# Optimization experiments

Hardware: AMD Instinct MI355X
Metric: run time of the kernel (lower is better)

The kernel has to match this reference:

```python
import jax, jax.numpy as jnp
import numpy as np

B, S, D, E, F, K = 2, 4096, 1024, 8, 2048, 2


def setup_inputs() -> dict:
    key = jax.random.key(0)
    k1, k2, k3, k4 = jax.random.split(key, 4)
    return {
        "inputs_raw": jax.random.normal(k1, (B, S, D), dtype=jnp.float32),
        "gate_w": jax.random.normal(k2, (D, E), dtype=jnp.float32) * (D ** -0.5),
        "w1": jax.random.normal(k3, (E, D, F), dtype=jnp.float32) * (D ** -0.5),
        "w2": jax.random.normal(k4, (E, F, D), dtype=jnp.float32) * (F ** -0.5),
        "top_k": K,
    }


def reference(inputs_raw, gate_w, w1, w2, top_k):
    ishape = inputs_raw.shape
    x = inputs_raw.reshape(-1, ishape[-1])                 # [T, D]
    n_experts = gate_w.shape[-1]

    # --- gating: top-k logits, softmax over the selected k (float32, like the torch code) ---
    logits = x @ gate_w                                    # [T, E]
    top_vals, top_idx = jax.lax.top_k(logits, top_k)       # [T, K]
    top_w = jax.nn.softmax(top_vals.astype(jnp.float32), axis=-1).astype(x.dtype)
    # dense combine weights [T, E]; zero for unselected experts
    combine = jnp.einsum("tk,tke->te", top_w,
                         jax.nn.one_hot(top_idx, n_experts, dtype=x.dtype))

    # --- experts: D -> F (SiLU) -> D, evaluated densely and combined with gate weights ---
    h = jax.nn.silu(jnp.einsum("td,edf->etf", x, w1))      # [E, T, F]
    y = jnp.einsum("etf,efd->etd", h, w2)                  # [E, T, D]
    out = jnp.einsum("te,etd->td", combine, y)             # [T, D]
    return out.reshape(ishape)
```

## Files before the change

kernel.cpp:

```cpp
#include <hip/hip_runtime.h>
#include <cstdint>
#include <cstddef>

#define T_TOK 8192
#define DIM   1024
#define NE    8
#define FF    2048
#define TOPK  2

typedef __bf16 bf16x8 __attribute__((ext_vector_type(8)));
typedef float  floatx4 __attribute__((ext_vector_type(4)));

__device__ __forceinline__ unsigned short f2bf(float f) {
  unsigned int u = __float_as_uint(f);
  unsigned int r = 0x7FFFu + ((u >> 16) & 1u);
  return (unsigned short)((u + r) >> 16);
}

__device__ __forceinline__ void gl_lds16(const void* g, void* l) {
  __builtin_amdgcn_global_load_lds(
      (__attribute__((address_space(1))) void*)g,
      (__attribute__((address_space(3))) void*)l,
      16, 0, 0);
}

__global__ __launch_bounds__(256) void transpose_bf16_kernel(
    const float* __restrict__ in, unsigned short* __restrict__ out,
    int R, int C)
{
  __shared__ float tile[32][33];
  int e  = blockIdx.z;
  int c0 = blockIdx.x * 32, r0 = blockIdx.y * 32;
  int tx = threadIdx.x & 31, ty = threadIdx.x >> 5;
  const float* inp = in + (size_t)e * R * C;
  unsigned short* op = out + (size_t)e * R * C;
  for (int i = 0; i < 4; ++i)
    tile[ty + i * 8][tx] = inp[(size_t)(r0 + ty + i * 8) * C + c0 + tx];
  __syncthreads();
  for (int i = 0; i < 4; ++i)
    op[(size_t)(c0 + ty + i * 8) * R + r0 + tx] = f2bf(tile[tx][ty + i * 8]);
}

__global__ __launch_bounds__(256) void gate_kernel(
    const float* __restrict__ x, const float* __restrict__ gw,
    unsigned short* __restrict__ xb, int* __restrict__ tokExp,
    float* __restrict__ tokW)
{
  __shared__ float gwT[NE][DIM];
  int tid = threadIdx.x;
  for (int i = tid; i < DIM * NE; i += 256) {
    int d = i >> 3, e = i & 7;
    gwT[e][d] = gw[i];
  }
  __syncthreads();

  int wv = tid >> 6, lane = tid & 63;
  int t = blockIdx.x * 4 + wv;
  const float* xrow = x + (size_t)t * DIM;
  unsigned short* xbrow = xb + (size_t)t * DIM;

  double acc[NE];
  for (int e = 0; e < NE; ++e) acc[e] = 0.0;

  for (int j = 0; j < 4; ++j) {
    float4 xv = ((const float4*)xrow)[j * 64 + lane];
    ushort4 s;
    s.x = f2bf(xv.x); s.y = f2bf(xv.y); s.z = f2bf(xv.z); s.w = f2bf(xv.w);
    ((ushort4*)xbrow)[j * 64 + lane] = s;
    double xd0 = (double)xv.x, xd1 = (double)xv.y;
    double xd2 = (double)xv.z, xd3 = (double)xv.w;
    for (int e = 0; e < NE; ++e) {
      float4 g = ((const float4*)&gwT[e][0])[j * 64 + lane];
      acc[e] += xd0 * (double)g.x + xd1 * (double)g.y +
                xd2 * (double)g.z + xd3 * (double)g.w;
    }
  }

  for (int s = 32; s > 0; s >>= 1)
    for (int e = 0; e < NE; ++e)
      acc[e] += __shfl_down(acc[e], s, 64);

  if (lane == 0) {
    int e0 = 0; double v0 = acc[0];
    for (int e = 1; e < NE; ++e) if (acc[e] > v0) { v0 = acc[e]; e0 = e; }
    int e1 = -1; double v1 = -1.0e300;
    for (int e = 0; e < NE; ++e) {
      if (e == e0) continue;
      if (acc[e] > v1) { v1 = acc[e]; e1 = e; }
    }
    float a = (float)v0, b = (float)v1;
    float eb = __expf(b - a);
    float den = 1.0f + eb;
    tokExp[t] = e0 | (e1 << 8);
    tokW[2 * t + 0] = 1.0f / den;
    tokW[2 * t + 1] = eb / den;
  }
}

__global__ __launch_bounds__(64) void assign_kernel(
    const int* __restrict__ tokExp, int* __restrict__ tokEnc,
    int* __restrict__ tIdx, int* __restrict__ cnt, int* __restrict__ off)
{
  int lane = threadIdx.x;
  unsigned long long below = (1ull << lane) - 1ull;
  int base[NE];
  for (int e = 0; e < NE; ++e) base[e] = 0;

  for (int it = 0; it < T_TOK / 64; ++it) {
    int t = it * 64 + lane;
    int enc = tokExp[t];
    int e0 = enc & 0xFF, e1 = (enc >> 8) & 0xFF;
    int s0 = 0, s1 = 0;
    for (int e = 0; e < NE; ++e) {
      unsigned long long m0 = __ballot(e0 == e);
      unsigned long long m1 = __ballot(e1 == e);
      if (e0 == e) s0 = base[e] + __popcll(m0 & below);
      if (e1 == e) s1 = base[e] + __popcll(m0) + __popcll(m1 & below);
      base[e] += __popcll(m0) + __popcll(m1);
    }
    tokEnc[2 * t + 0] = (e0 << 16) | s0;
    tokEnc[2 * t + 1] = (e1 << 16) | s1;
    tIdx[e0 * T_TOK + s0] = t;
    tIdx[e1 * T_TOK + s1] = t;
  }

  if (lane == 0) {
    int a = 0;
    for (int e = 0; e < NE; ++e) { cnt[e] = base[e]; off[e] = a; a += base[e]; }
    off[NE] = a;
  }
}

__global__ __launch_bounds__(256, 4) void gemm1_kernel(
    const unsigned short* __restrict__ xb,
    const unsigned short* __restrict__ w1t,
    unsigned short* __restrict__ h,
    const int* __restrict__ tIdx, const int* __restrict__ cnt,
    const int* __restrict__ off)
{
  int g = blockIdx.x;
  int e = g & 7;
  int b = g >> 3;
  int phase = b >> 9;
  int m = (b >> 3) & 63;
  int nl = b & 7;
  int count = cnt[e];
  int r0 = m * 128;
  if (r0 >= count) return;
  int n0 = (phase * 8 + nl) * 128;

  __shared__ __align__(16) unsigned short As[8][128][8];
  __shared__ __align__(16) unsigned short Bs[8][128][8];

  int tid = threadIdx.x, lane = tid & 63, w = tid >> 6;
  int wr = w >> 1, wc = w & 1;
  int quad = lane >> 4, li = lane & 15;

  const unsigned short* ag[2];
  const unsigned short* bg[2];
  for (int c = 0; c < 2; ++c) {
    int mm = c * 64 + lane;
    int r = r0 + mm; if (r > count - 1) r = count - 1;
    ag[c] = xb + (size_t)tIdx[e * T_TOK + r] * DIM;
    bg[c] = w1t + ((size_t)e * FF + (n0 + mm)) * DIM;
  }

  floatx4 acc[4][4];
  for (int mi = 0; mi < 4; ++mi)
    for (int ni = 0; ni < 4; ++ni)
      for (int q = 0; q < 4; ++q) acc[mi][ni][q] = 0.0f;

  for (int k0 = 0; k0 < DIM; k0 += 64) {
    __syncthreads();
    for (int kk = 0; kk < 2; ++kk) {
      int kq = w + kk * 4;
      gl_lds16(ag[0] + k0 + kq * 8, &As[kq][0][0]);
      gl_lds16(ag[1] + k0 + kq * 8, &As[kq][64][0]);
      gl_lds16(bg[0] + k0 + kq * 8, &Bs[kq][0][0]);
      gl_lds16(bg[1] + k0 + kq * 8, &Bs[kq][64][0]);
    }
    __syncthreads();
    for (int ks = 0; ks < 2; ++ks) {
      bf16x8 af[4], bf[4];
      for (int mi = 0; mi < 4; ++mi)
        af[mi] = *(const bf16x8*)&As[ks * 4 + quad][wr * 64 + mi * 16 + li][0];
      for (int ni = 0; ni < 4; ++ni)
        bf[ni] = *(const bf16x8*)&Bs[ks * 4 + quad][wc * 64 + ni * 16 + li][0];
      for (int mi = 0; mi < 4; ++mi)
        for (int ni = 0; ni < 4; ++ni)
          acc[mi][ni] = __builtin_amdgcn_mfma_f32_16x16x32_bf16(
              af[mi], bf[ni], acc[mi][ni], 0, 0, 0);
    }
  }

  size_t hb = (size_t)off[e];
  for (int mi = 0; mi < 4; ++mi) {
    int rowb = wr * 64 + mi * 16 + quad * 4;
    for (int rr = 0; rr < 4; ++rr) {
      int r = r0 + rowb + rr;
      if (r >= count) continue;
      unsigned short* hrow = h + (hb + r) * FF + n0 + wc * 64 + li;
      for (int ni = 0; ni < 4; ++ni) {
        float v = acc[mi][ni][rr];
        float s = v / (1.0f + __expf(-v));
        hrow[ni * 16] = f2bf(s);
      }
    }
  }
}

__global__ __launch_bounds__(256, 4) void gemm2_kernel(
    const unsigned short* __restrict__ h,
    const unsigned short* __restrict__ w2t,
    float* __restrict__ yv,
    const int* __restrict__ cnt, const int* __restrict__ off)
{
  int g = blockIdx.x;
  int e = g & 7;
  int b = g >> 3;
  int phase = b >> 8;
  int m = (b >> 2) & 63;
  int nl = b & 3;
  int count = cnt[e];
  int r0 = m * 128;
  if (r0 >= count) return;
  int n0 = (phase * 4 + nl) * 128;

  __shared__ __align__(16) unsigned short As[8][128][8];
  __shared__ __align__(16) unsigned short Bs[8][128][8];

  int tid = threadIdx.x, lane = tid & 63, w = tid >> 6;
  int wr = w >> 1, wc = w & 1;
  int quad = lane >> 4, li = lane & 15;
  size_t yb = (size_t)off[e];

  const unsigned short* ag[2];
  const unsigned short* bg[2];
  for (int c = 0; c < 2; ++c) {
    int mm = c * 64 + lane;
    int r = r0 + mm; if (r > count - 1) r = count - 1;
    ag[c] = h + (yb + r) * FF;
    bg[c] = w2t + ((size_t)e * DIM + (n0 + mm)) * FF;
  }

  floatx4 acc[4][4];
  for (int mi = 0; mi < 4; ++mi)
    for (int ni = 0; ni < 4; ++ni)
      for (int q = 0; q < 4; ++q) acc[mi][ni][q] = 0.0f;

  for (int k0 = 0; k0 < FF; k0 += 64) {
    __syncthreads();
    for (int kk = 0; kk < 2; ++kk) {
      int kq = w + kk * 4;
      gl_lds16(ag[0] + k0 + kq * 8, &As[kq][0][0]);
      gl_lds16(ag[1] + k0 + kq * 8, &As[kq][64][0]);
      gl_lds16(bg[0] + k0 + kq * 8, &Bs[kq][0][0]);
      gl_lds16(bg[1] + k0 + kq * 8, &Bs[kq][64][0]);
    }
    __syncthreads();
    for (int ks = 0; ks < 2; ++ks) {
      bf16x8 af[4], bf[4];
      for (int mi = 0; mi < 4; ++mi)
        af[mi] = *(const bf16x8*)&As[ks * 4 + quad][wr * 64 + mi * 16 + li][0];
      for (int ni = 0; ni < 4; ++ni)
        bf[ni] = *(const bf16x8*)&Bs[ks * 4 + quad][wc * 64 + ni * 16 + li][0];
      for (int mi = 0; mi < 4; ++mi)
        for (int ni = 0; ni < 4; ++ni)
          acc[mi][ni] = __builtin_amdgcn_mfma_f32_16x16x32_bf16(
              af[mi], bf[ni], acc[mi][ni], 0, 0, 0);
    }
  }

  for (int mi = 0; mi < 4; ++mi) {
    int rowb = wr * 64 + mi * 16 + quad * 4;
    for (int rr = 0; rr < 4; ++rr) {
      int r = r0 + rowb + rr;
      if (r >= count) continue;
      float* yrow = yv + (yb + r) * DIM + n0 + wc * 64 + li;
      for (int ni = 0; ni < 4; ++ni)
        yrow[ni * 16] = acc[mi][ni][rr];
    }
  }
}

__global__ __launch_bounds__(256) void combine_kernel(
    const float* __restrict__ yv, const int* __restrict__ tokEnc,
    const float* __restrict__ tokW, const int* __restrict__ off,
    float* __restrict__ out)
{
  int t = blockIdx.x;
  int i = threadIdx.x;
  int enc0 = tokEnc[2 * t + 0], enc1 = tokEnc[2 * t + 1];
  float w0 = tokW[2 * t + 0], w1 = tokW[2 * t + 1];
  size_t row0 = (size_t)off[enc0 >> 16] + (enc0 & 0xFFFF);
  size_t row1 = (size_t)off[enc1 >> 16] + (enc1 & 0xFFFF);
  float4 a = ((const float4*)(yv + row0 * DIM))[i];
  float4 b = ((const float4*)(yv + row1 * DIM))[i];
  float4 o;
  o.x = w0 * a.x + w1 * b.x;
  o.y = w0 * a.y + w1 * b.y;
  o.z = w0 * a.z + w1 * b.z;
  o.w = w0 * a.w + w1 * b.w;
  ((float4*)(out + (size_t)t * DIM))[i] = o;
}

extern "C" void kernel_launch(void* const* d_in, const int* in_sizes, int n_in,
                              void* d_out, int out_size, void* d_ws, size_t ws_size,
                              hipStream_t stream)
{
  const float* x  = (const float*)d_in[0];
  const float* gw = (const float*)d_in[1];
  const float* w1 = (const float*)d_in[2];
  const float* w2 = (const float*)d_in[3];
  float* out = (float*)d_out;

  size_t o = 0;
  auto alloc = [&](size_t bytes) {
    void* p = (char*)d_ws + o;
    o += (bytes + 255) & ~(size_t)255;
    return p;
  };
  unsigned short* xb   = (unsigned short*)alloc((size_t)T_TOK * DIM * 2);
  unsigned short* w1t  = (unsigned short*)alloc((size_t)NE * DIM * FF * 2);
  unsigned short* w2t  = (unsigned short*)alloc((size_t)NE * DIM * FF * 2);
  unsigned short* hbuf = (unsigned short*)alloc((size_t)T_TOK * TOPK * FF * 2);
  float*          yv   = (float*)alloc((size_t)T_TOK * TOPK * DIM * 4);
  int*   tIdx   = (int*)alloc((size_t)NE * T_TOK * 4);
  int*   tokEnc = (int*)alloc((size_t)2 * T_TOK * 4);
  float* tokW   = (float*)alloc((size_t)2 * T_TOK * 4);
  int*   tokExp = (int*)alloc((size_t)T_TOK * 4);
  int*   cnt    = (int*)alloc((size_t)NE * 4);
  int*   off    = (int*)alloc((size_t)(NE + 1) * 4);

  transpose_bf16_kernel<<<dim3(FF / 32, DIM / 32, NE), 256, 0, stream>>>(w1, w1t, DIM, FF);
  transpose_bf16_kernel<<<dim3(DIM / 32, FF / 32, NE), 256, 0, stream>>>(w2, w2t, FF, DIM);

  gate_kernel<<<T_TOK / 4, 256, 0, stream>>>(x, gw, xb, tokExp, tokW);
  assign_kernel<<<1, 64, 0, stream>>>(tokExp, tokEnc, tIdx, cnt, off);

  gemm1_kernel<<<8192, 256, 0, stream>>>(xb, w1t, hbuf, tIdx, cnt, off);
  gemm2_kernel<<<4096, 256, 0, stream>>>(hbuf, w2t, yv, cnt, off);
  combine_kernel<<<T_TOK, 256, 0, stream>>>(yv, tokEnc, tokW, off, out);
}
```

Baseline: 607.3 us.

## Parallelize expert assignment with atomics and double-buffer GEMM LDS tiles

The single-wave serial assign kernel becomes a multi-block kernel in which each wave reserves slots per expert through atomicAdd on counters zeroed in the gate kernel. Per-expert offsets are now recomputed from the counts inside the consumer kernels, and the precomputed offset array is removed. Both expert GEMMs double-buffer their LDS tiles so the next k-slice's global-to-LDS loads overlap the current MFMA work, with one barrier per iteration instead of two. Launch bounds drop to two blocks per CU to fit the doubled shared memory. Token order within an expert is now nondeterministic, and lowering occupancy may offset part of the overlap gain.

```diff
diff --git a/kernel.cpp b/kernel.cpp
--- a/kernel.cpp
+++ b/kernel.cpp
@@ -44,10 +44,11 @@
 __global__ __launch_bounds__(256) void gate_kernel(
     const float* __restrict__ x, const float* __restrict__ gw,
     unsigned short* __restrict__ xb, int* __restrict__ tokExp,
-    float* __restrict__ tokW)
+    float* __restrict__ tokW, int* __restrict__ cnt)
 {
   __shared__ float gwT[NE][DIM];
   int tid = threadIdx.x;
+  if (blockIdx.x == 0 && tid < NE) cnt[tid] = 0;
   for (int i = tid; i < DIM * NE; i += 256) {
     int d = i >> 3, e = i & 7;
     gwT[e][d] = gw[i];
@@ -97,46 +98,38 @@
   }
 }
 
-__global__ __launch_bounds__(64) void assign_kernel(
+__global__ __launch_bounds__(256) void assign_kernel(
     const int* __restrict__ tokExp, int* __restrict__ tokEnc,
-    int* __restrict__ tIdx, int* __restrict__ cnt, int* __restrict__ off)
-{
-  int lane = threadIdx.x;
+    int* __restrict__ tIdx, int* __restrict__ cnt)
+{
+  int t = blockIdx.x * 256 + threadIdx.x;
+  int lane = threadIdx.x & 63;
   unsigned long long below = (1ull << lane) - 1ull;
-  int base[NE];
-  for (int e = 0; e < NE; ++e) base[e] = 0;
-
-  for (int it = 0; it < T_TOK / 64; ++it) {
-    int t = it * 64 + lane;
-    int enc = tokExp[t];
-    int e0 = enc & 0xFF, e1 = (enc >> 8) & 0xFF;
-    int s0 = 0, s1 = 0;
-    for (int e = 0; e < NE; ++e) {
-      unsigned long long m0 = __ballot(e0 == e);
-      unsigned long long m1 = __ballot(e1 == e);
-      if (e0 == e) s0 = base[e] + __popcll(m0 & below);
-      if (e1 == e) s1 = base[e] + __popcll(m0) + __popcll(m1 & below);
-      base[e] += __popcll(m0) + __popcll(m1);
-    }
-    tokEnc[2 * t + 0] = (e0 << 16) | s0;
-    tokEnc[2 * t + 1] = (e1 << 16) | s1;
-    tIdx[e0 * T_TOK + s0] = t;
-    tIdx[e1 * T_TOK + s1] = t;
-  }
-
-  if (lane == 0) {
-    int a = 0;
-    for (int e = 0; e < NE; ++e) { cnt[e] = base[e]; off[e] = a; a += base[e]; }
-    off[NE] = a;
-  }
-}
-
-__global__ __launch_bounds__(256, 4) void gemm1_kernel(
+  int enc = tokExp[t];
+  int e0 = enc & 0xFF, e1 = (enc >> 8) & 0xFF;
+  int s0 = 0, s1 = 0;
+  for (int e = 0; e < NE; ++e) {
+    unsigned long long m0 = __ballot(e0 == e);
+    unsigned long long m1 = __ballot(e1 == e);
+    int c0 = __popcll(m0), c1 = __popcll(m1);
+    int base = 0;
+    if (lane == 0 && (c0 + c1) > 0)
+      base = atomicAdd(&cnt[e], c0 + c1);
+    base = __shfl(base, 0, 64);
+    if (e0 == e) s0 = base + __popcll(m0 & below);
+    if (e1 == e) s1 = base + c0 + __popcll(m1 & below);
+  }
+  tokEnc[2 * t + 0] = (e0 << 16) | s0;
+  tokEnc[2 * t + 1] = (e1 << 16) | s1;
+  tIdx[e0 * T_TOK + s0] = t;
+  tIdx[e1 * T_TOK + s1] = t;
+}
+
+__global__ __launch_bounds__(256, 2) void gemm1_kernel(
     const unsigned short* __restrict__ xb,
     const unsigned short* __restrict__ w1t,
     unsigned short* __restrict__ h,
-    const int* __restrict__ tIdx, const int* __restrict__ cnt,
-    const int* __restrict__ off)
+    const int* __restrict__ tIdx, const int* __restrict__ cnt)
 {
   int g = blockIdx.x;
   int e = g & 7;
@@ -149,8 +142,8 @@
   if (r0 >= count) return;
   int n0 = (phase * 8 + nl) * 128;
 
-  __shared__ __align__(16) unsigned short As[8][128][8];
-  __shared__ __align__(16) unsigned short Bs[8][128][8];
+  __shared__ __align__(16) unsigned short As[2][8][128][8];
+  __shared__ __align__(16) unsigned short Bs[2][8][128][8];
 
   int tid = threadIdx.x, lane = tid & 63, w = tid >> 6;
   int wr = w >> 1, wc = w & 1;
@@ -170,30 +163,38 @@
     for (int ni = 0; ni < 4; ++ni)
       for (int q = 0; q < 4; ++q) acc[mi][ni][q] = 0.0f;
 
-  for (int k0 = 0; k0 < DIM; k0 += 64) {
-    __syncthreads();
+  auto stage = [&](int buf, int k0) {
     for (int kk = 0; kk < 2; ++kk) {
       int kq = w + kk * 4;
-      gl_lds16(ag[0] + k0 + kq * 8, &As[kq][0][0]);
-      gl_lds16(ag[1] + k0 + kq * 8, &As[kq][64][0]);
-      gl_lds16(bg[0] + k0 + kq * 8, &Bs[kq][0][0]);
-      gl_lds16(bg[1] + k0 + kq * 8, &Bs[kq][64][0]);
-    }
-    __syncthreads();
+      gl_lds16(ag[0] + k0 + kq * 8, &As[buf][kq][0][0]);
+      gl_lds16(ag[1] + k0 + kq * 8, &As[buf][kq][64][0]);
+      gl_lds16(bg[0] + k0 + kq * 8, &Bs[buf][kq][0][0]);
+      gl_lds16(bg[1] + k0 + kq * 8, &Bs[buf][kq][64][0]);
+    }
+  };
+
+  stage(0, 0);
+  __syncthreads();
+  int cur = 0;
+  for (int k0 = 0; k0 < DIM; k0 += 64) {
+    if (k0 + 64 < DIM) stage(cur ^ 1, k0 + 64);
     for (int ks = 0; ks < 2; ++ks) {
       bf16x8 af[4], bf[4];
       for (int mi = 0; mi < 4; ++mi)
-        af[mi] = *(const bf16x8*)&As[ks * 4 + quad][wr * 64 + mi * 16 + li][0];
+        af[mi] = *(const bf16x8*)&As[cur][ks * 4 + quad][wr * 64 + mi * 16 + li][0];
       for (int ni = 0; ni < 4; ++ni)
-        bf[ni] = *(const bf16x8*)&Bs[ks * 4 + quad][wc * 64 + ni * 16 + li][0];
+        bf[ni] = *(const bf16x8*)&Bs[cur][ks * 4 + quad][wc * 64 + ni * 16 + li][0];
       for (int mi = 0; mi < 4; ++mi)
         for (int ni = 0; ni < 4; ++ni)
           acc[mi][ni] = __builtin_amdgcn_mfma_f32_16x16x32_bf16(
               af[mi], bf[ni], acc[mi][ni], 0, 0, 0);
     }
-  }
-
-  size_t hb = (size_t)off[e];
+    __syncthreads();
+    cur ^= 1;
+  }
+
+  size_t hb = 0;
+  for (int i = 0; i < e; ++i) hb += cnt[i];
   for (int mi = 0; mi < 4; ++mi) {
     int rowb = wr * 64 + mi * 16 + quad * 4;
     for (int rr = 0; rr < 4; ++rr) {
@@ -209,11 +210,11 @@
   }
 }
 
-__global__ __launch_bounds__(256, 4) void gemm2_kernel(
+__global__ __launch_bounds__(256, 2) void gemm2_kernel(
     const unsigned short* __restrict__ h,
     const unsigned short* __restrict__ w2t,
     float* __restrict__ yv,
-    const int* __restrict__ cnt, const int* __restrict__ off)
+    const int* __restrict__ cnt)
 {
   int g = blockIdx.x;
   int e = g & 7;
@@ -226,13 +227,14 @@
   if (r0 >= count) return;
   int n0 = (phase * 4 + nl) * 128;
 
-  __shared__ __align__(16) unsigned short As[8][128][8];
-  __shared__ __align__(16) unsigned short Bs[8][128][8];
+  __shared__ __align__(16) unsigned short As[2][8][128][8];
+  __shared__ __align__(16) unsigned short Bs[2][8][128][8];
 
   int tid = threadIdx.x, lane = tid & 63, w = tid >> 6;
   int wr = w >> 1, wc = w & 1;
   int quad = lane >> 4, li = lane & 15;
-  size_t yb = (size_t)off[e];
+  size_t yb = 0;
+  for (int i = 0; i < e; ++i) yb += cnt[i];
 
   const unsigned short* ag[2];
   const unsigned short* bg[2];
@@ -248,27 +250,34 @@
     for (int ni = 0; ni < 4; ++ni)
       for (int q = 0; q < 4; ++q) acc[mi][ni][q] = 0.0f;
 
-  for (int k0 = 0; k0 < FF; k0 += 64) {
-    __syncthreads();
+  auto stage = [&](int buf, int k0) {
     for (int kk = 0; kk < 2; ++kk) {
       int kq = w + kk * 4;
-      gl_lds16(ag[0] + k0 + kq * 8, &As[kq][0][0]);
-      gl_lds16(ag[1] + k0 + kq * 8, &As[kq][64][0]);
-      gl_lds16(bg[0] + k0 + kq * 8, &Bs[kq][0][0]);
-      gl_lds16(bg[1] + k0 + kq * 8, &Bs[kq][64][0]);
-    }
-    __syncthreads();
+      gl_lds16(ag[0] + k0 + kq * 8, &As[buf][kq][0][0]);
+      gl_lds16(ag[1] + k0 + kq * 8, &As[buf][kq][64][0]);
+      gl_lds16(bg[0] + k0 + kq * 8, &Bs[buf][kq][0][0]);
+      gl_lds16(bg[1] + k0 + kq * 8, &Bs[buf][kq][64][0]);
+    }
+  };
+
+  stage(0, 0);
+  __syncthreads();
+  int cur = 0;
+  for (int k0 = 0; k0 < FF; k0 += 64) {
+    if (k0 + 64 < FF) stage(cur ^ 1, k0 + 64);
     for (int ks = 0; ks < 2; ++ks) {
       bf16x8 af[4], bf[4];
       for (int mi = 0; mi < 4; ++mi)
-        af[mi] = *(const bf16x8*)&As[ks * 4 + quad][wr * 64 + mi * 16 + li][0];
+        af[mi] = *(const bf16x8*)&As[cur][ks * 4 + quad][wr * 64 + mi * 16 + li][0];
       for (int ni = 0; ni < 4; ++ni)
-        bf[ni] = *(const bf16x8*)&Bs[ks * 4 + quad][wc * 64 + ni * 16 + li][0];
+        bf[ni] = *(const bf16x8*)&Bs[cur][ks * 4 + quad][wc * 64 + ni * 16 + li][0];
       for (int mi = 0; mi < 4; ++mi)
         for (int ni = 0; ni < 4; ++ni)
           acc[mi][ni] = __builtin_amdgcn_mfma_f32_16x16x32_bf16(
               af[mi], bf[ni], acc[mi][ni], 0, 0, 0);
     }
+    __syncthreads();
+    cur ^= 1;
   }
 
   for (int mi = 0; mi < 4; ++mi) {
@@ -285,22 +294,29 @@
 
 __global__ __launch_bounds__(256) void combine_kernel(
     const float* __restrict__ yv, const int* __restrict__ tokEnc,
-    const float* __restrict__ tokW, const int* __restrict__ off,
+    const float* __restrict__ tokW, const int* __restrict__ cnt,
     float* __restrict__ out)
 {
   int t = blockIdx.x;
   int i = threadIdx.x;
   int enc0 = tokEnc[2 * t + 0], enc1 = tokEnc[2 * t + 1];
   float w0 = tokW[2 * t + 0], w1 = tokW[2 * t + 1];
-  size_t row0 = (size_t)off[enc0 >> 16] + (enc0 & 0xFFFF);
-  size_t row1 = (size_t)off[enc1 >> 16] + (enc1 & 0xFFFF);
-  float4 a = ((const float4*)(yv + row0 * DIM))[i];
-  float4 b = ((const float4*)(yv + row1 * DIM))[i];
+  int x0 = enc0 >> 16, x1 = enc1 >> 16;
+  int off0 = 0, off1 = 0, a = 0;
+  for (int e = 0; e < NE; ++e) {
+    if (e == x0) off0 = a;
+    if (e == x1) off1 = a;
+    a += cnt[e];
+  }
+  size_t row0 = (size_t)off0 + (enc0 & 0xFFFF);
+  size_t row1 = (size_t)off1 + (enc1 & 0xFFFF);
+  float4 va = ((const float4*)(yv + row0 * DIM))[i];
+  float4 vb = ((const float4*)(yv + row1 * DIM))[i];
   float4 o;
-  o.x = w0 * a.x + w1 * b.x;
-  o.y = w0 * a.y + w1 * b.y;
-  o.z = w0 * a.z + w1 * b.z;
-  o.w = w0 * a.w + w1 * b.w;
+  o.x = w0 * va.x + w1 * vb.x;
+  o.y = w0 * va.y + w1 * vb.y;
+  o.z = w0 * va.z + w1 * vb.z;
+  o.w = w0 * va.w + w1 * vb.w;
   ((float4*)(out + (size_t)t * DIM))[i] = o;
 }
 
@@ -330,15 +346,14 @@
   float* tokW   = (float*)alloc((size_t)2 * T_TOK * 4);
   int*   tokExp = (int*)alloc((size_t)T_TOK * 4);
   int*   cnt    = (int*)alloc((size_t)NE * 4);
-  int*   off    = (int*)alloc((size_t)(NE + 1) * 4);
 
   transpose_bf16_kernel<<<dim3(FF / 32, DIM / 32, NE), 256, 0, stream>>>(w1, w1t, DIM, FF);
   transpose_bf16_kernel<<<dim3(DIM / 32, FF / 32, NE), 256, 0, stream>>>(w2, w2t, FF, DIM);
 
-  gate_kernel<<<T_TOK / 4, 256, 0, stream>>>(x, gw, xb, tokExp, tokW);
-  assign_kernel<<<1, 64, 0, stream>>>(tokExp, tokEnc, tIdx, cnt, off);
-
-  gemm1_kernel<<<8192, 256, 0, stream>>>(xb, w1t, hbuf, tIdx, cnt, off);
-  gemm2_kernel<<<4096, 256, 0, stream>>>(hbuf, w2t, yv, cnt, off);
-  combine_kernel<<<T_TOK, 256, 0, stream>>>(yv, tokEnc, tokW, off, out);
-}
+  gate_kernel<<<T_TOK / 4, 256, 0, stream>>>(x, gw, xb, tokExp, tokW, cnt);
+  assign_kernel<<<T_TOK / 256, 256, 0, stream>>>(tokExp, tokEnc, tIdx, cnt);
+
+  gemm1_kernel<<<8192, 256, 0, stream>>>(xb, w1t, hbuf, tIdx, cnt);
+  gemm2_kernel<<<4096, 256, 0, stream>>>(hbuf, w2t, yv, cnt);
+  combine_kernel<<<T_TOK, 256, 0, stream>>>(yv, tokEnc, tokW, cnt, out);
+}
```

Result: faster. 584.3 us (-3.8%).
